# Performance work log

Measured on AMD Instinct MI355X. Metric: run time of the kernel, lower is better.

The kernel has to match this reference:

```python
import jax, jax.numpy as jnp
import numpy as np
from jax import lax

KERNEL = 31
SMOOTH = 0.001
PAD = KERNEL // 2


def _avg_pool2d(x):
    # torch F.avg_pool2d(kernel=31, stride=1, padding=15, count_include_pad=True):
    # sum over 31x31 window with zero padding, then divide by 31*31 always.
    s = lax.reduce_window(
        x, 0.0, lax.add,
        window_dimensions=(1, 1, KERNEL, KERNEL),
        window_strides=(1, 1, 1, 1),
        padding=((0, 0), (0, 0), (PAD, PAD), (PAD, PAD)),
    )
    return s / (KERNEL * KERNEL)


def setup_inputs() -> dict:
    key = jax.random.key(0)
    k1, k2 = jax.random.split(key)
    B, C, H, W = 32, 1, 1024, 1024
    output = jax.random.normal(k1, (B, C, H, W), dtype=jnp.float32)
    target = jax.random.uniform(k2, (B, C, H, W), dtype=jnp.float32)
    return {"output": output, "target": target}


def reference(output, target):
    out = jax.nn.sigmoid(output)
    weight = 1.0 + 5.0 * jnp.abs(_avg_pool2d(target) - target)  # [B,C,H,W]
    inter = jnp.sum(out * target * weight, axis=(2, 3)).reshape(-1, 1)      # [B*C,1]
    mask_sum = jnp.sum((target + out) * weight, axis=(2, 3)).reshape(-1, 1)  # [B*C,1]
    loss = 1.0 - (2.0 * inter + SMOOTH) / (mask_sum + SMOOTH)
    return jnp.mean(loss)
```

## Files before the change

kernel.cpp:

```cpp
#include <hip/hip_runtime.h>
#include <math.h>


namespace {
constexpr int Bn = 32;
constexpr int Hn = 1024;
constexpr int Wn = 1024;
constexpr int Rn = 15;
constexpr int TX = 256;
constexpr int YS = 128;
constexpr int NCOL = TX + 32;
constexpr int PHYSW = (NCOL / 8) * 12;
constexpr float INV_KK = 1.0f / 961.0f;
}

__device__ __forceinline__ int phys(int i) { return i + ((i >> 3) << 2); }

__device__ __forceinline__ float ldg0(const float* p, int y, int x) {
    return (y >= 0 && y < Hn && x >= 0 && x < Wn) ? p[(size_t)y * Wn + x] : 0.0f;
}

__global__ __launch_bounds__(256, 2)
void dice_main(const float* __restrict__ logits, const float* __restrict__ tgt,
               float* __restrict__ acc)
{
    __shared__ __align__(16) float vbuf[8 * PHYSW];
    __shared__ float red[8];

    const int bid = blockIdx.x;
    const int b   = bid >> 5;
    const int rem = bid & 31;
    const int x0  = (rem >> 3) * TX;
    const int y0  = (rem & 7) * YS;
    const int t   = threadIdx.x;

    const float* tb = tgt    + (size_t)b * Hn * Wn;
    const float* ob = logits + (size_t)b * Hn * Wn;

    const int  col0 = x0 - Rn + t;
    const bool has2 = (t < 32);
    const int  col1 = col0 + 256;

    float vs0 = 0.0f, vs1 = 0.0f;
    for (int yy = y0 - Rn; yy <= y0 + Rn; ++yy) {
        vs0 += ldg0(tb, yy, col0);
        if (has2) vs1 += ldg0(tb, yy, col1);
    }

    float acc_i = 0.0f, acc_m = 0.0f;

    for (int it = 0; it < YS / 8; ++it) {
        const int ya = y0 + it * 8;

        #pragma unroll
        for (int r = 0; r < 8; ++r) {
            const int yr = ya + r;
            if (yr != y0) {
                vs0 += ldg0(tb, yr + Rn, col0) - ldg0(tb, yr - Rn - 1, col0);
                if (has2) vs1 += ldg0(tb, yr + Rn, col1) - ldg0(tb, yr - Rn - 1, col1);
            }
            vbuf[r * PHYSW + phys(t)] = vs0;
            if (has2) vbuf[r * PHYSW + phys(256 + t)] = vs1;
        }
        __syncthreads();

        {
            const int r = t >> 5;
            const int j = t & 31;
            const int yrow = ya + r;
            const float* vrow = &vbuf[r * PHYSW];

            float w[40];
            #pragma unroll
            for (int k = 0; k < 10; ++k) {
                const int l = (j << 3) + (k << 2);
                const float4 q = *(const float4*)&vrow[phys(l)];
                w[4 * k + 0] = q.x; w[4 * k + 1] = q.y;
                w[4 * k + 2] = q.z; w[4 * k + 3] = q.w;
            }

            const int xb = x0 + (j << 3);
            const float4* tq = (const float4*)(tb + (size_t)yrow * Wn + xb);
            const float4 t0 = tq[0], t1 = tq[1];
            const float4* oq = (const float4*)(ob + (size_t)yrow * Wn + xb);
            const float4 o0 = oq[0], o1 = oq[1];
            const float tc[8] = {t0.x, t0.y, t0.z, t0.w, t1.x, t1.y, t1.z, t1.w};
            const float oc[8] = {o0.x, o0.y, o0.z, o0.w, o1.x, o1.y, o1.z, o1.w};

            float s = 0.0f;
            #pragma unroll
            for (int c = 0; c < 31; ++c) s += w[c];
            #pragma unroll
            for (int m = 0; m < 8; ++m) {
                if (m > 0) s += w[30 + m] - w[m - 1];
                const float avg = s * INV_KK;
                const float wt  = 1.0f + 5.0f * fabsf(avg - tc[m]);
                const float sg  = 1.0f / (1.0f + __expf(-oc[m]));
                acc_i += sg * tc[m] * wt;
                acc_m += (tc[m] + sg) * wt;
            }
        }
        __syncthreads();
    }

    #pragma unroll
    for (int off = 32; off > 0; off >>= 1) {
        acc_i += __shfl_down(acc_i, off);
        acc_m += __shfl_down(acc_m, off);
    }
    const int lane = t & 63;
    const int wv   = t >> 6;
    if (lane == 0) { red[wv * 2] = acc_i; red[wv * 2 + 1] = acc_m; }
    __syncthreads();
    if (t == 0) {
        atomicAdd(&acc[2 * b],     red[0] + red[2] + red[4] + red[6]);
        atomicAdd(&acc[2 * b + 1], red[1] + red[3] + red[5] + red[7]);
    }
}

__global__ void dice_final(const float* __restrict__ acc, float* __restrict__ out)
{
    const int t = threadIdx.x;
    float l = 0.0f;
    if (t < Bn) {
        const float I = acc[2 * t];
        const float M = acc[2 * t + 1];
        l = 1.0f - (2.0f * I + 0.001f) / (M + 0.001f);
    }
    #pragma unroll
    for (int off = 32; off > 0; off >>= 1) l += __shfl_down(l, off);
    if (t == 0) out[0] = l * (1.0f / 32.0f);
}

extern "C" void kernel_launch(void* const* d_in, const int* in_sizes, int n_in,
                              void* d_out, int out_size, void* d_ws, size_t ws_size,
                              hipStream_t stream)
{
    const float* logits = (const float*)d_in[0];
    const float* target = (const float*)d_in[1];
    float* acc = (float*)d_ws;

    hipMemsetAsync(d_ws, 0, 64 * sizeof(float), stream);
    dice_main<<<dim3(Bn * 32), dim3(256), 0, stream>>>(logits, target, acc);
    dice_final<<<dim3(1), dim3(64), 0, stream>>>(acc, (float*)d_out);
}
```

Measured before the change: 337.7 us.

## Prefetch next row block's target and logits loads into registers, raise occupancy hint

Result: faster. 318.0 us (-5.8%).

```diff
diff --git a/kernel.cpp b/kernel.cpp
--- a/kernel.cpp
+++ b/kernel.cpp
@@ -9,6 +9,7 @@
 constexpr int Rn = 15;
 constexpr int TX = 256;
 constexpr int YS = 128;
+constexpr int NB = YS / 8;
 constexpr int NCOL = TX + 32;
 constexpr int PHYSW = (NCOL / 8) * 12;
 constexpr float INV_KK = 1.0f / 961.0f;
@@ -16,11 +17,11 @@
 
 __device__ __forceinline__ int phys(int i) { return i + ((i >> 3) << 2); }
 
-__device__ __forceinline__ float ldg0(const float* p, int y, int x) {
-    return (y >= 0 && y < Hn && x >= 0 && x < Wn) ? p[(size_t)y * Wn + x] : 0.0f;
+__device__ __forceinline__ float ldcol(const float* p, int y, int col, bool xok) {
+    return (xok && (unsigned)y < (unsigned)Hn) ? p[(size_t)y * Wn + col] : 0.0f;
 }
 
-__global__ __launch_bounds__(256, 2)
+__global__ __launch_bounds__(256, 4)
 void dice_main(const float* __restrict__ logits, const float* __restrict__ tgt,
                float* __restrict__ acc)
 {
@@ -40,56 +41,84 @@
     const int  col0 = x0 - Rn + t;
     const bool has2 = (t < 32);
     const int  col1 = col0 + 256;
+    const bool xok0 = (col0 >= 0) && (col0 < Wn);
+    const bool xok1 = (col1 >= 0) && (col1 < Wn);
+    const int  pt   = phys(t);
+    const int  pt2  = phys(256 + t);
+
+    const int rr = t >> 5;
+    const int jj = t & 31;
+    const int xb = x0 + (jj << 3);
 
     float vs0 = 0.0f, vs1 = 0.0f;
     for (int yy = y0 - Rn; yy <= y0 + Rn; ++yy) {
-        vs0 += ldg0(tb, yy, col0);
-        if (has2) vs1 += ldg0(tb, yy, col1);
+        vs0 += ldcol(tb, yy, col0, xok0);
+        if (has2) vs1 += ldcol(tb, yy, col1, xok1);
+    }
+
+    float pA[8], qA[8];
+    #pragma unroll
+    for (int r = 0; r < 8; ++r) {
+        pA[r] = ldcol(tb, y0 + r + Rn, col0, xok0);
+        qA[r] = has2 ? ldcol(tb, y0 + r + Rn, col1, xok1) : 0.0f;
+    }
+    float4 ct0, ct1, co0, co1;
+    {
+        const float* tp = tb + (size_t)(y0 + rr) * Wn + xb;
+        const float* op = ob + (size_t)(y0 + rr) * Wn + xb;
+        ct0 = ((const float4*)tp)[0]; ct1 = ((const float4*)tp)[1];
+        co0 = ((const float4*)op)[0]; co1 = ((const float4*)op)[1];
     }
 
     float acc_i = 0.0f, acc_m = 0.0f;
 
-    for (int it = 0; it < YS / 8; ++it) {
+    for (int it = 0; it < NB; ++it) {
         const int ya = y0 + it * 8;
 
         #pragma unroll
         for (int r = 0; r < 8; ++r) {
             const int yr = ya + r;
-            if (yr != y0) {
-                vs0 += ldg0(tb, yr + Rn, col0) - ldg0(tb, yr - Rn - 1, col0);
-                if (has2) vs1 += ldg0(tb, yr + Rn, col1) - ldg0(tb, yr - Rn - 1, col1);
+            if (it > 0 || r > 0) {
+                vs0 += pA[r] - ldcol(tb, yr - Rn - 1, col0, xok0);
+                if (has2) vs1 += qA[r] - ldcol(tb, yr - Rn - 1, col1, xok1);
             }
-            vbuf[r * PHYSW + phys(t)] = vs0;
-            if (has2) vbuf[r * PHYSW + phys(256 + t)] = vs1;
+            vbuf[r * PHYSW + pt] = vs0;
+            if (has2) vbuf[r * PHYSW + pt2] = vs1;
         }
         __syncthreads();
 
+        float4 nt0, nt1, no0, no1;
+        if (it + 1 < NB) {
+            #pragma unroll
+            for (int r = 0; r < 8; ++r) {
+                pA[r] = ldcol(tb, ya + 8 + r + Rn, col0, xok0);
+                if (has2) qA[r] = ldcol(tb, ya + 8 + r + Rn, col1, xok1);
+            }
+            const float* tp = tb + (size_t)(ya + 8 + rr) * Wn + xb;
+            const float* op = ob + (size_t)(ya + 8 + rr) * Wn + xb;
+            nt0 = ((const float4*)tp)[0]; nt1 = ((const float4*)tp)[1];
+            no0 = ((const float4*)op)[0]; no1 = ((const float4*)op)[1];
+        }
+
         {
-            const int r = t >> 5;
-            const int j = t & 31;
-            const int yrow = ya + r;
-            const float* vrow = &vbuf[r * PHYSW];
-
+            const float* vrow = &vbuf[rr * PHYSW];
             float w[40];
             #pragma unroll
             for (int k = 0; k < 10; ++k) {
-                const int l = (j << 3) + (k << 2);
-                const float4 q = *(const float4*)&vrow[phys(l)];
+                const float4 q = *(const float4*)&vrow[phys((jj << 3) + (k << 2))];
                 w[4 * k + 0] = q.x; w[4 * k + 1] = q.y;
                 w[4 * k + 2] = q.z; w[4 * k + 3] = q.w;
             }
 
-            const int xb = x0 + (j << 3);
-            const float4* tq = (const float4*)(tb + (size_t)yrow * Wn + xb);
-            const float4 t0 = tq[0], t1 = tq[1];
-            const float4* oq = (const float4*)(ob + (size_t)yrow * Wn + xb);
-            const float4 o0 = oq[0], o1 = oq[1];
-            const float tc[8] = {t0.x, t0.y, t0.z, t0.w, t1.x, t1.y, t1.z, t1.w};
-            const float oc[8] = {o0.x, o0.y, o0.z, o0.w, o1.x, o1.y, o1.z, o1.w};
+            const float tc[8] = {ct0.x, ct0.y, ct0.z, ct0.w, ct1.x, ct1.y, ct1.z, ct1.w};
+            const float oc[8] = {co0.x, co0.y, co0.z, co0.w, co1.x, co1.y, co1.z, co1.w};
 
-            float s = 0.0f;
+            float s0 = 0.0f, s1 = 0.0f, s2 = 0.0f, s3 = 0.0f;
             #pragma unroll
-            for (int c = 0; c < 31; ++c) s += w[c];
+            for (int c = 0; c < 28; c += 4) {
+                s0 += w[c]; s1 += w[c + 1]; s2 += w[c + 2]; s3 += w[c + 3];
+            }
+            float s = (s0 + s1) + (s2 + s3) + w[28] + w[29] + w[30];
             #pragma unroll
             for (int m = 0; m < 8; ++m) {
                 if (m > 0) s += w[30 + m] - w[m - 1];
@@ -100,6 +129,8 @@
                 acc_m += (tc[m] + sg) * wt;
             }
         }
+
+        if (it + 1 < NB) { ct0 = nt0; ct1 = nt1; co0 = no0; co1 = no1; }
         __syncthreads();
     }
 
```
